# Optimization experiments

Measured on AMD Instinct MI355X. Metric: run time of the kernel, lower is better.

## Reference

```python
import jax, jax.numpy as jnp
import numpy as np

B, S, D, H = 2, 2048, 1024, 16
HD = D // H
MASK_VALUE = -1000000.0


def setup_inputs() -> dict:
    key = jax.random.key(0)
    ks = jax.random.split(key, 8)
    scale = 1.0 / np.sqrt(D)
    return {
        "Q": jax.random.normal(ks[0], (B, S, D), jnp.float32),
        "K": jax.random.normal(ks[1], (B, S, D), jnp.float32),
        "V": jax.random.normal(ks[2], (B, S, D), jnp.float32),
        "valid_lens": jax.random.randint(ks[3], (B,), 0, S).astype(jnp.int32),
        "Wq": jax.random.normal(ks[4], (D, D), jnp.float32) * scale,
        "Wk": jax.random.normal(ks[5], (D, D), jnp.float32) * scale,
        "Wv": jax.random.normal(ks[6], (D, D), jnp.float32) * scale,
        "Wo": jax.random.normal(ks[7], (D, D), jnp.float32) * scale,
    }


def _split_heads(x):
    # [B,S,D] -> [B,H,S,HD]
    return x.reshape(B, S, H, HD).transpose(0, 2, 1, 3)


def reference(Q, K, V, valid_lens, Wq, Wk, Wv, Wo):
    q = _split_heads(Q @ Wq)
    k = _split_heads(K @ Wk)
    v = _split_heads(V @ Wv)
    # scores: [B,H,Sq,Sk]
    scores = jnp.einsum("bhqd,bhkd->bhqk", q, k) / jnp.sqrt(jnp.float32(HD))
    # mask key positions >= valid_len (per batch, broadcast over heads/queries)
    key_pos = jnp.arange(S)  # [Sk]
    mask = key_pos[None, None, None, :] < valid_lens[:, None, None, None]
    scores = jnp.where(mask, scores, MASK_VALUE)
    attn = jax.nn.softmax(scores, axis=-1)
    out = jnp.einsum("bhqk,bhkd->bhqd", attn, v)  # [B,H,S,HD]
    out = out.transpose(0, 2, 1, 3).reshape(B, S, D)
    return out @ Wo
```

## Files before the change

### kernel.cpp

```cpp
#include <hip/hip_runtime.h>
#include <stdint.h>

#define B_ 2
#define S_ 2048
#define D_ 1024
#define H_ 16
#define HD_ 64
#define MG_ (B_*S_)
#define MASKV -1000000.0f
#define LP_ 72
#define LO_ 68
#define M2_ 17.3f
#define QSCALE_ (0.125f * 1.44269504088896f)

typedef __bf16 bf16;
typedef bf16 bf16x8 __attribute__((ext_vector_type(8)));
typedef bf16 bf16x4 __attribute__((ext_vector_type(4)));
typedef float f32x4 __attribute__((ext_vector_type(4)));

#define MFMA(a, b, c) __builtin_amdgcn_mfma_f32_16x16x32_bf16(a, b, c, 0, 0, 0)

__device__ __forceinline__ void gl_lds16(const bf16* g, bf16* l) {
  __builtin_amdgcn_global_load_lds((const __attribute__((address_space(1))) void*)g,
                                   (__attribute__((address_space(3))) void*)l, 16, 0, 0);
}

__global__ __launch_bounds__(256) void wcast_kernel(const float* __restrict__ W0, const float* __restrict__ W1,
                                                    const float* __restrict__ W2, const float* __restrict__ W3,
                                                    bf16* __restrict__ T) {
  const float* W = blockIdx.z == 0 ? W0 : blockIdx.z == 1 ? W1 : blockIdx.z == 2 ? W2 : W3;
  bf16* Tz = T + (size_t)blockIdx.z * D_ * D_;
  __shared__ float tile[32][33];
  int tx = threadIdx.x & 31, ty = threadIdx.x >> 5;
  int bn = blockIdx.x * 32, bk = blockIdx.y * 32;
#pragma unroll
  for (int i = 0; i < 32; i += 8)
    tile[ty + i][tx] = W[(size_t)(bk + ty + i) * D_ + bn + tx];
  __syncthreads();
#pragma unroll
  for (int i = 0; i < 32; i += 8)
    Tz[(size_t)(bn + ty + i) * D_ + bk + tx] = (bf16)tile[tx][ty + i];
}

__global__ __launch_bounds__(256) void qkvcast_kernel(const float* __restrict__ Qin, const float* __restrict__ Kin,
                                                      const float* __restrict__ Vin, bf16* __restrict__ qb,
                                                      bf16* __restrict__ kb, bf16* __restrict__ vb) {
  int t = blockIdx.y;
  const float* src = t == 0 ? Qin : t == 1 ? Kin : Vin;
  bf16* dst = t == 0 ? qb : t == 1 ? kb : vb;
  float sc = t == 0 ? QSCALE_ : 1.0f;
  size_t base4 = (size_t)blockIdx.x * 2048 + threadIdx.x;
#pragma unroll
  for (int j = 0; j < 8; ++j) {
    size_t i4 = base4 + (size_t)j * 256;
    float4 v = *(const float4*)&src[i4 * 4];
    bf16x4 bv; bv[0] = (bf16)(v.x * sc); bv[1] = (bf16)(v.y * sc);
    bv[2] = (bf16)(v.z * sc); bv[3] = (bf16)(v.w * sc);
    *(bf16x4*)&dst[i4 * 4] = bv;
  }
}

__global__ __launch_bounds__(256) void proj_gemm_b(const bf16* __restrict__ qb, const bf16* __restrict__ kb,
                                                   const bf16* __restrict__ vb, const bf16* __restrict__ WT,
                                                   bf16* __restrict__ qh, bf16* __restrict__ kh,
                                                   bf16* __restrict__ vT) {
  __shared__ alignas(16) bf16 Sa[128 * 32];
  __shared__ alignas(16) bf16 Sw[128 * 32];
  int mode = blockIdx.y;
  int bx = blockIdx.x;
  int i1 = (bx & 7) + ((bx >> 6) << 3);
  int i2 = (bx >> 3) & 7;
  int tid = threadIdx.x, lane = tid & 63, w = tid >> 6;
  int wm = w >> 1, wn = w & 1, ml = lane & 15, quad = lane >> 4;
  int l4 = lane >> 2, k8 = (lane & 3) * 8;
  f32x4 acc[4][4] = {};

  const bf16* Tok = mode == 0 ? qb : mode == 1 ? kb : vb;
  const bf16* Hp = WT + (size_t)mode * D_ * D_;
  int frow0 = i1 * 128, hrow0 = i2 * 128;
  bf16* Xs = (mode < 2) ? Sa : Sw;
  bf16* Ys = (mode < 2) ? Sw : Sa;

  for (int kk = 0; kk < D_; kk += 32) {
    __syncthreads();
#pragma unroll
    for (int j = 0; j < 2; ++j) {
      int chunk = w * 2 + j;
      gl_lds16(&Tok[(size_t)(frow0 + chunk * 16 + l4) * D_ + kk + k8], &Sa[chunk * 16 * 32]);
      gl_lds16(&Hp[(size_t)(hrow0 + chunk * 16 + l4) * D_ + kk + k8], &Sw[chunk * 16 * 32]);
    }
    __syncthreads();
    bf16x8 af[4], bfr[4];
#pragma unroll
    for (int mt = 0; mt < 4; ++mt) af[mt] = *(bf16x8*)&Xs[(wm * 64 + mt * 16 + ml) * 32 + quad * 8];
#pragma unroll
    for (int nt = 0; nt < 4; ++nt) bfr[nt] = *(bf16x8*)&Ys[(wn * 64 + nt * 16 + ml) * 32 + quad * 8];
#pragma unroll
    for (int mt = 0; mt < 4; ++mt)
#pragma unroll
      for (int nt = 0; nt < 4; ++nt)
        acc[mt][nt] = MFMA(af[mt], bfr[nt], acc[mt][nt]);
  }

  if (mode < 2) {
    bf16* dst = mode ? kh : qh;
    int m0 = i1 * 128, n0 = i2 * 128;
#pragma unroll
    for (int mt = 0; mt < 4; ++mt)
#pragma unroll
      for (int nt = 0; nt < 4; ++nt)
#pragma unroll
        for (int r = 0; r < 4; ++r) {
          int m = m0 + wm * 64 + mt * 16 + quad * 4 + r;
          int n = n0 + wn * 64 + nt * 16 + ml;
          int b = m >> 11, s = m & (S_ - 1), h = n >> 6, hd = n & 63;
          dst[(((size_t)(b * H_ + h)) * S_ + s) * HD_ + hd] = (bf16)acc[mt][nt][r];
        }
  } else {
    int m0 = i2 * 128, n0 = i1 * 128;
#pragma unroll
    for (int mt = 0; mt < 4; ++mt)
#pragma unroll
      for (int nt = 0; nt < 4; ++nt)
#pragma unroll
        for (int r = 0; r < 4; ++r) {
          int dcol = m0 + wm * 64 + mt * 16 + quad * 4 + r;
          int n = n0 + wn * 64 + nt * 16 + ml;
          int b = n >> 11, s = n & (S_ - 1), h = dcol >> 6, hd = dcol & 63;
          vT[(((size_t)(b * H_ + h)) * HD_ + hd) * S_ + s] = (bf16)acc[mt][nt][r];
        }
  }
}

__global__ __launch_bounds__(256) void proj_gemm(const float* __restrict__ Qin, const float* __restrict__ Kin,
                                                 const float* __restrict__ Vin, const bf16* __restrict__ WT,
                                                 bf16* __restrict__ qh, bf16* __restrict__ kh,
                                                 bf16* __restrict__ vT) {
  __shared__ alignas(16) bf16 Asf[128 * 32];
  __shared__ alignas(16) bf16 Ash[128 * 32];
  int mode = blockIdx.y;
  int bx = blockIdx.x;
  int i1 = (bx & 7) + ((bx >> 6) << 3);
  int i2 = (bx >> 3) & 7;
  int tid = threadIdx.x, lane = tid & 63, w = tid >> 6;
  int wm = w >> 1, wn = w & 1, ml = lane & 15, quad = lane >> 4;
  int rr = tid >> 3, c4 = (tid & 7) * 4;
  int l4 = lane >> 2, k8 = (lane & 3) * 8;
  f32x4 acc[4][4] = {};

  const float* Fp = mode == 0 ? Qin : mode == 1 ? Kin : Vin;
  const bf16* Hp = WT + (size_t)mode * D_ * D_;
  int frow0 = i1 * 128, hrow0 = i2 * 128;
  bf16* Xs = (mode < 2) ? Asf : Ash;
  bf16* Ys = (mode < 2) ? Ash : Asf;

  for (int kk = 0; kk < D_; kk += 32) {
    __syncthreads();
#pragma unroll
    for (int j = 0; j < 2; ++j) {
      int chunk = w * 2 + j;
      gl_lds16(&Hp[(size_t)(hrow0 + chunk * 16 + l4) * D_ + kk + k8], &Ash[chunk * 16 * 32]);
    }
#pragma unroll
    for (int p = 0; p < 4; ++p) {
      float4 v = *(const float4*)&Fp[(size_t)(frow0 + rr + p * 32) * D_ + kk + c4];
      bf16x4 bv; bv[0] = (bf16)v.x; bv[1] = (bf16)v.y; bv[2] = (bf16)v.z; bv[3] = (bf16)v.w;
      *(bf16x4*)&Asf[(rr + p * 32) * 32 + c4] = bv;
    }
    __syncthreads();
    bf16x8 af[4], bfr[4];
#pragma unroll
    for (int mt = 0; mt < 4; ++mt) af[mt] = *(bf16x8*)&Xs[(wm * 64 + mt * 16 + ml) * 32 + quad * 8];
#pragma unroll
    for (int nt = 0; nt < 4; ++nt) bfr[nt] = *(bf16x8*)&Ys[(wn * 64 + nt * 16 + ml) * 32 + quad * 8];
#pragma unroll
    for (int mt = 0; mt < 4; ++mt)
#pragma unroll
      for (int nt = 0; nt < 4; ++nt)
        acc[mt][nt] = MFMA(af[mt], bfr[nt], acc[mt][nt]);
  }

  if (mode < 2) {
    bf16* dst = mode ? kh : qh;
    float oscale = mode ? 1.0f : QSCALE_;
    int m0 = i1 * 128, n0 = i2 * 128;
#pragma unroll
    for (int mt = 0; mt < 4; ++mt)
#pragma unroll
      for (int nt = 0; nt < 4; ++nt)
#pragma unroll
        for (int r = 0; r < 4; ++r) {
          int m = m0 + wm * 64 + mt * 16 + quad * 4 + r;
          int n = n0 + wn * 64 + nt * 16 + ml;
          int b = m >> 11, s = m & (S_ - 1), h = n >> 6, hd = n & 63;
          dst[(((size_t)(b * H_ + h)) * S_ + s) * HD_ + hd] = (bf16)(acc[mt][nt][r] * oscale);
        }
  } else {
    int m0 = i2 * 128, n0 = i1 * 128;
#pragma unroll
    for (int mt = 0; mt < 4; ++mt)
#pragma unroll
      for (int nt = 0; nt < 4; ++nt)
#pragma unroll
        for (int r = 0; r < 4; ++r) {
          int dcol = m0 + wm * 64 + mt * 16 + quad * 4 + r;
          int n = n0 + wn * 64 + nt * 16 + ml;
          int b = n >> 11, s = n & (S_ - 1), h = dcol >> 6, hd = dcol & 63;
          vT[(((size_t)(b * H_ + h)) * HD_ + hd) * S_ + s] = (bf16)acc[mt][nt][r];
        }
  }
}

__global__ __launch_bounds__(256) void attn_kernel(const bf16* __restrict__ qh, const bf16* __restrict__ kh,
                                                   const bf16* __restrict__ vT, const int* __restrict__ vlen,
                                                   bf16* __restrict__ ctx) {
  __shared__ alignas(16) char ldsraw[35328];
  bf16* Ps = (bf16*)ldsraw;
  float* Om = (float*)ldsraw;
  float* Lv = (float*)(ldsraw + 34816);

  int tid = threadIdx.x, lane = tid & 63, w = tid >> 6;
  int ml = lane & 15, quad = lane >> 4;
  int wq = w >> 1, wk = w & 1;
  int bx = blockIdx.x;
  int bh = (bx & 7) + ((bx >> 8) << 3);
  int qt = (bx >> 3) & 31;
  int b = bh >> 4, h = bh & 15;
  const bf16* qbase = qh + ((size_t)bh * S_ + qt * 64 + wq * 32) * HD_;
  const bf16* kbase = kh + (size_t)bh * S_ * HD_;
  const bf16* vbase = vT + (size_t)bh * HD_ * S_;
  int valid = vlen[b];
  int nkt = (valid == 0) ? (S_ / 64) : ((valid + 63) >> 6);

  bf16x8 aq[2][2];
#pragma unroll
  for (int mt = 0; mt < 2; ++mt)
#pragma unroll
    for (int half = 0; half < 2; ++half)
      aq[mt][half] = *(const bf16x8*)&qbase[(mt * 16 + ml) * HD_ + half * 32 + quad * 8];

  bf16 onev = (bf16)1.0f;
  bf16x8 ones = {onev, onev, onev, onev, onev, onev, onev, onev};

  f32x4 o[2][4] = {};
  f32x4 lacc[2] = {};

  bf16* Pw = Ps + (size_t)w * 32 * LP_;

  for (int kt = wk; kt < nkt; kt += 2) {
    const bf16* kp = kbase + (size_t)kt * 64 * HD_;
    bool tail = (kt * 64 + 64 > valid);
    bf16x8 bk[4][2];
#pragma unroll
    for (int nt = 0; nt < 4; ++nt)
#pragma unroll
      for (int half = 0; half < 2; ++half)
        bk[nt][half] = *(const bf16x8*)&kp[(nt * 16 + ml) * HD_ + half * 32 + quad * 8];

#pragma unroll
    for (int mt = 0; mt < 2; ++mt) {
      f32x4 sc[4];
#pragma unroll
      for (int nt = 0; nt < 4; ++nt) {
        f32x4 c = {};
        c = MFMA(aq[mt][0], bk[nt][0], c);
        c = MFMA(aq[mt][1], bk[nt][1], c);
        sc[nt] = c;
      }
#pragma unroll
      for (int r = 0; r < 4; ++r) {
#pragma unroll
        for (int nt = 0; nt < 4; ++nt) {
          float s = sc[nt][r];
          if (tail) {
            int col = kt * 64 + nt * 16 + ml;
            if (col >= valid) s = MASKV;
          }
          if (valid == 0) s = 0.f;
          float p = exp2f(s - M2_);
          Pw[(mt * 16 + quad * 4 + r) * LP_ + nt * 16 + ml] = (bf16)p;
        }
      }
    }
#pragma unroll
    for (int ks = 0; ks < 2; ++ks) {
      bf16x8 bv[4];
#pragma unroll
      for (int ht = 0; ht < 4; ++ht)
        bv[ht] = *(const bf16x8*)&vbase[(size_t)(ht * 16 + ml) * S_ + kt * 64 + ks * 32 + quad * 8];
#pragma unroll
      for (int mt = 0; mt < 2; ++mt) {
        bf16x8 ap = *(bf16x8*)&Pw[(mt * 16 + ml) * LP_ + ks * 32 + quad * 8];
        lacc[mt] = MFMA(ap, ones, lacc[mt]);
#pragma unroll
        for (int ht = 0; ht < 4; ++ht) o[mt][ht] = MFMA(ap, bv[ht], o[mt][ht]);
      }
    }
  }

  __syncthreads();
#pragma unroll
  for (int mt = 0; mt < 2; ++mt) {
#pragma unroll
    for (int r = 0; r < 4; ++r) {
      int rl = mt * 16 + quad * 4 + r;
#pragma unroll
      for (int ht = 0; ht < 4; ++ht)
        Om[(w * 32 + rl) * LO_ + ht * 16 + ml] = o[mt][ht][r];
      if (ml == 0) Lv[w * 32 + rl] = lacc[mt][r];
    }
  }
  __syncthreads();
#pragma unroll 4
  for (int rr = 0; rr < 16; ++rr) {
    int rg = w * 16 + rr;
    int wqs = rg >> 5, rl = rg & 31;
    int s0 = (wqs * 2) * 32 + rl, s1 = (wqs * 2 + 1) * 32 + rl;
    float ls = Lv[s0] + Lv[s1];
    float ov = Om[s0 * LO_ + lane] + Om[s1 * LO_ + lane];
    ctx[((size_t)b * S_ + qt * 64 + rg) * D_ + h * 64 + lane] = (bf16)(ov / ls);
  }
}

__global__ __launch_bounds__(256) void out_gemm(const bf16* __restrict__ ctx, const bf16* __restrict__ WoT,
                                                float* __restrict__ out) {
  __shared__ alignas(16) bf16 As[128 * 32];
  __shared__ alignas(16) bf16 Bs[64 * 32];
  int bx = blockIdx.x;
  int mt8 = (bx & 7) + ((bx >> 7) << 3);
  int ntile = (bx >> 3) & 15;
  int tid = threadIdx.x, lane = tid & 63, w = tid >> 6;
  int wm = w >> 1, wn = w & 1, ml = lane & 15, quad = lane >> 4;
  int l4 = lane >> 2, k8 = (lane & 3) * 8;
  int m0 = mt8 * 128, n0 = ntile * 64;
  f32x4 acc[4][2] = {};
  for (int kk = 0; kk < D_; kk += 32) {
    __syncthreads();
#pragma unroll
    for (int j = 0; j < 2; ++j) {
      int chunk = w * 2 + j;
      gl_lds16(&ctx[(size_t)(m0 + chunk * 16 + l4) * D_ + kk + k8], &As[chunk * 16 * 32]);
    }
    gl_lds16(&WoT[(size_t)(n0 + w * 16 + l4) * D_ + kk + k8], &Bs[w * 16 * 32]);
    __syncthreads();
    bf16x8 af[4], bfr[2];
#pragma unroll
    for (int mt = 0; mt < 4; ++mt) af[mt] = *(bf16x8*)&As[(wm * 64 + mt * 16 + ml) * 32 + quad * 8];
#pragma unroll
    for (int nt = 0; nt < 2; ++nt) bfr[nt] = *(bf16x8*)&Bs[(wn * 32 + nt * 16 + ml) * 32 + quad * 8];
#pragma unroll
    for (int mt = 0; mt < 4; ++mt)
#pragma unroll
      for (int nt = 0; nt < 2; ++nt)
        acc[mt][nt] = MFMA(af[mt], bfr[nt], acc[mt][nt]);
  }
#pragma unroll
  for (int mt = 0; mt < 4; ++mt)
#pragma unroll
    for (int nt = 0; nt < 2; ++nt)
#pragma unroll
      for (int r = 0; r < 4; ++r) {
        int m = m0 + wm * 64 + mt * 16 + quad * 4 + r;
        int n = n0 + wn * 32 + nt * 16 + ml;
        out[(size_t)m * D_ + n] = acc[mt][nt][r];
      }
}

extern "C" void kernel_launch(void* const* d_in, const int* in_sizes, int n_in,
                              void* d_out, int out_size, void* d_ws, size_t ws_size,
                              hipStream_t stream) {
  const float* Q = (const float*)d_in[0];
  const float* K = (const float*)d_in[1];
  const float* V = (const float*)d_in[2];
  const int* vl = (const int*)d_in[3];
  const float* Wq = (const float*)d_in[4];
  const float* Wk = (const float*)d_in[5];
  const float* Wv = (const float*)d_in[6];
  const float* Wo = (const float*)d_in[7];
  char* ws = (char*)d_ws;
  bf16* WT  = (bf16*)ws;
  bf16* qh  = (bf16*)(ws + 8ull * 1024 * 1024);
  bf16* kh  = (bf16*)(ws + 16ull * 1024 * 1024);
  bf16* vT  = (bf16*)(ws + 24ull * 1024 * 1024);
  bf16* ctx = (bf16*)(ws + 32ull * 1024 * 1024);
  bf16* qb  = ctx;
  bf16* kb  = (bf16*)(ws + 40ull * 1024 * 1024);
  bf16* vb  = (bf16*)(ws + 48ull * 1024 * 1024);
  float* out = (float*)d_out;

  bool big = ws_size >= 56ull * 1024 * 1024;

  wcast_kernel<<<dim3(32, 32, 4), 256, 0, stream>>>(Wq, Wk, Wv, Wo, WT);
  if (big) {
    qkvcast_kernel<<<dim3(512, 3), 256, 0, stream>>>(Q, K, V, qb, kb, vb);
    proj_gemm_b<<<dim3(256, 3), 256, 0, stream>>>(qb, kb, vb, WT, qh, kh, vT);
  } else {
    proj_gemm<<<dim3(256, 3), 256, 0, stream>>>(Q, K, V, WT, qh, kh, vT);
  }
  attn_kernel<<<dim3(1024), 256, 0, stream>>>(qh, kh, vT, vl, ctx);
  out_gemm<<<dim3(512), 256, 0, stream>>>(ctx, WT + 3ull * D_ * D_, out);
}
```

Baseline: 222.9 us.

## Fuse weight and input casts into one kernel, skip K/V rows beyond valid length

Merges the weight transpose-cast and the Q/K/V bf16 cast into a single front kernel launch, removing one launch and letting both kinds of work share the GPU. The cast and the K/V projection GEMM now read valid_lens and skip token tiles past the rounded-up valid key length, since the attention kernel never reads those keys or values. This avoids wasted projection compute and memory traffic for masked keys, but relies on the attention kernel honouring the same kneed bound, including the valid==0 case treated as full length.

```diff
diff --git a/kernel.cpp b/kernel.cpp
--- a/kernel.cpp
+++ b/kernel.cpp
@@ -25,6 +25,130 @@
                                    (__attribute__((address_space(3))) void*)l, 16, 0, 0);
 }
 
+__device__ __forceinline__ int kneed_of(int valid) {
+  return (valid == 0) ? S_ : ((valid + 63) & ~63);
+}
+
+__global__ __launch_bounds__(256) void front_kernel(const float* __restrict__ W0, const float* __restrict__ W1,
+                                                    const float* __restrict__ W2, const float* __restrict__ W3,
+                                                    bf16* __restrict__ T, const float* __restrict__ Qin,
+                                                    const float* __restrict__ Kin, const float* __restrict__ Vin,
+                                                    bf16* __restrict__ qb, bf16* __restrict__ kb,
+                                                    bf16* __restrict__ vb, const int* __restrict__ vlen) {
+  __shared__ float tile[32][33];
+  int z = blockIdx.y;
+  if (z < 4) {
+    const float* W = z == 0 ? W0 : z == 1 ? W1 : z == 2 ? W2 : W3;
+    bf16* Tz = T + (size_t)z * D_ * D_;
+    int tx = threadIdx.x & 31, ty = threadIdx.x >> 5;
+    int bn = (blockIdx.x & 31) * 32, bk = (blockIdx.x >> 5) * 32;
+#pragma unroll
+    for (int i = 0; i < 32; i += 8)
+      tile[ty + i][tx] = W[(size_t)(bk + ty + i) * D_ + bn + tx];
+    __syncthreads();
+#pragma unroll
+    for (int i = 0; i < 32; i += 8)
+      Tz[(size_t)(bn + ty + i) * D_ + bk + tx] = (bf16)tile[tx][ty + i];
+  } else {
+    int t = z - 4;
+    const float* src = t == 0 ? Qin : t == 1 ? Kin : Vin;
+    bf16* dst = t == 0 ? qb : t == 1 ? kb : vb;
+    float sc = t == 0 ? QSCALE_ : 1.0f;
+    if (t) {
+      int m0 = blockIdx.x * 4;
+      int b = m0 >> 11, s0 = m0 & (S_ - 1);
+      int kneed128 = (kneed_of(vlen[b]) + 127) & ~127;
+      if (s0 >= kneed128) return;
+    }
+    size_t base4 = (size_t)blockIdx.x * 1024 + threadIdx.x;
+#pragma unroll
+    for (int j = 0; j < 4; ++j) {
+      size_t i4 = base4 + (size_t)j * 256;
+      float4 v = *(const float4*)&src[i4 * 4];
+      bf16x4 bv; bv[0] = (bf16)(v.x * sc); bv[1] = (bf16)(v.y * sc);
+      bv[2] = (bf16)(v.z * sc); bv[3] = (bf16)(v.w * sc);
+      *(bf16x4*)&dst[i4 * 4] = bv;
+    }
+  }
+}
+
+__global__ __launch_bounds__(256) void proj_gemm_b(const bf16* __restrict__ qb, const bf16* __restrict__ kb,
+                                                   const bf16* __restrict__ vb, const bf16* __restrict__ WT,
+                                                   bf16* __restrict__ qh, bf16* __restrict__ kh,
+                                                   bf16* __restrict__ vT, const int* __restrict__ vlen) {
+  __shared__ alignas(16) bf16 Sa[128 * 32];
+  __shared__ alignas(16) bf16 Sw[128 * 32];
+  int mode = blockIdx.y;
+  int bx = blockIdx.x;
+  int i1 = (bx & 7) + ((bx >> 6) << 3);
+  int i2 = (bx >> 3) & 7;
+  if (mode >= 1) {
+    int m0tok = i1 * 128;
+    int b = m0tok >> 11, s0 = m0tok & (S_ - 1);
+    if (s0 >= kneed_of(vlen[b])) return;
+  }
+  int tid = threadIdx.x, lane = tid & 63, w = tid >> 6;
+  int wm = w >> 1, wn = w & 1, ml = lane & 15, quad = lane >> 4;
+  int l4 = lane >> 2, k8 = (lane & 3) * 8;
+  f32x4 acc[4][4] = {};
+
+  const bf16* Tok = mode == 0 ? qb : mode == 1 ? kb : vb;
+  const bf16* Hp = WT + (size_t)mode * D_ * D_;
+  int frow0 = i1 * 128, hrow0 = i2 * 128;
+  bf16* Xs = (mode < 2) ? Sa : Sw;
+  bf16* Ys = (mode < 2) ? Sw : Sa;
+
+  for (int kk = 0; kk < D_; kk += 32) {
+    __syncthreads();
+#pragma unroll
+    for (int j = 0; j < 2; ++j) {
+      int chunk = w * 2 + j;
+      gl_lds16(&Tok[(size_t)(frow0 + chunk * 16 + l4) * D_ + kk + k8], &Sa[chunk * 16 * 32]);
+      gl_lds16(&Hp[(size_t)(hrow0 + chunk * 16 + l4) * D_ + kk + k8], &Sw[chunk * 16 * 32]);
+    }
+    __syncthreads();
+    bf16x8 af[4], bfr[4];
+#pragma unroll
+    for (int mt = 0; mt < 4; ++mt) af[mt] = *(bf16x8*)&Xs[(wm * 64 + mt * 16 + ml) * 32 + quad * 8];
+#pragma unroll
+    for (int nt = 0; nt < 4; ++nt) bfr[nt] = *(bf16x8*)&Ys[(wn * 64 + nt * 16 + ml) * 32 + quad * 8];
+#pragma unroll
+    for (int mt = 0; mt < 4; ++mt)
+#pragma unroll
+      for (int nt = 0; nt < 4; ++nt)
+        acc[mt][nt] = MFMA(af[mt], bfr[nt], acc[mt][nt]);
+  }
+
+  if (mode < 2) {
+    bf16* dst = mode ? kh : qh;
+    int m0 = i1 * 128, n0 = i2 * 128;
+#pragma unroll
+    for (int mt = 0; mt < 4; ++mt)
+#pragma unroll
+      for (int nt = 0; nt < 4; ++nt)
+#pragma unroll
+        for (int r = 0; r < 4; ++r) {
+          int m = m0 + wm * 64 + mt * 16 + quad * 4 + r;
+          int n = n0 + wn * 64 + nt * 16 + ml;
+          int b = m >> 11, s = m & (S_ - 1), h = n >> 6, hd = n & 63;
+          dst[(((size_t)(b * H_ + h)) * S_ + s) * HD_ + hd] = (bf16)acc[mt][nt][r];
+        }
+  } else {
+    int m0 = i2 * 128, n0 = i1 * 128;
+#pragma unroll
+    for (int mt = 0; mt < 4; ++mt)
+#pragma unroll
+      for (int nt = 0; nt < 4; ++nt)
+#pragma unroll
+        for (int r = 0; r < 4; ++r) {
+          int dcol = m0 + wm * 64 + mt * 16 + quad * 4 + r;
+          int n = n0 + wn * 64 + nt * 16 + ml;
+          int b = n >> 11, s = n & (S_ - 1), h = dcol >> 6, hd = dcol & 63;
+          vT[(((size_t)(b * H_ + h)) * HD_ + hd) * S_ + s] = (bf16)acc[mt][nt][r];
+        }
+  }
+}
+
 __global__ __launch_bounds__(256) void wcast_kernel(const float* __restrict__ W0, const float* __restrict__ W1,
                                                     const float* __restrict__ W2, const float* __restrict__ W3,
                                                     bf16* __restrict__ T) {
@@ -40,96 +164,6 @@
 #pragma unroll
   for (int i = 0; i < 32; i += 8)
     Tz[(size_t)(bn + ty + i) * D_ + bk + tx] = (bf16)tile[tx][ty + i];
-}
-
-__global__ __launch_bounds__(256) void qkvcast_kernel(const float* __restrict__ Qin, const float* __restrict__ Kin,
-                                                      const float* __restrict__ Vin, bf16* __restrict__ qb,
-                                                      bf16* __restrict__ kb, bf16* __restrict__ vb) {
-  int t = blockIdx.y;
-  const float* src = t == 0 ? Qin : t == 1 ? Kin : Vin;
-  bf16* dst = t == 0 ? qb : t == 1 ? kb : vb;
-  float sc = t == 0 ? QSCALE_ : 1.0f;
-  size_t base4 = (size_t)blockIdx.x * 2048 + threadIdx.x;
-#pragma unroll
-  for (int j = 0; j < 8; ++j) {
-    size_t i4 = base4 + (size_t)j * 256;
-    float4 v = *(const float4*)&src[i4 * 4];
-    bf16x4 bv; bv[0] = (bf16)(v.x * sc); bv[1] = (bf16)(v.y * sc);
-    bv[2] = (bf16)(v.z * sc); bv[3] = (bf16)(v.w * sc);
-    *(bf16x4*)&dst[i4 * 4] = bv;
-  }
-}
-
-__global__ __launch_bounds__(256) void proj_gemm_b(const bf16* __restrict__ qb, const bf16* __restrict__ kb,
-                                                   const bf16* __restrict__ vb, const bf16* __restrict__ WT,
-                                                   bf16* __restrict__ qh, bf16* __restrict__ kh,
-                                                   bf16* __restrict__ vT) {
-  __shared__ alignas(16) bf16 Sa[128 * 32];
-  __shared__ alignas(16) bf16 Sw[128 * 32];
-  int mode = blockIdx.y;
-  int bx = blockIdx.x;
-  int i1 = (bx & 7) + ((bx >> 6) << 3);
-  int i2 = (bx >> 3) & 7;
-  int tid = threadIdx.x, lane = tid & 63, w = tid >> 6;
-  int wm = w >> 1, wn = w & 1, ml = lane & 15, quad = lane >> 4;
-  int l4 = lane >> 2, k8 = (lane & 3) * 8;
-  f32x4 acc[4][4] = {};
-
-  const bf16* Tok = mode == 0 ? qb : mode == 1 ? kb : vb;
-  const bf16* Hp = WT + (size_t)mode * D_ * D_;
-  int frow0 = i1 * 128, hrow0 = i2 * 128;
-  bf16* Xs = (mode < 2) ? Sa : Sw;
-  bf16* Ys = (mode < 2) ? Sw : Sa;
-
-  for (int kk = 0; kk < D_; kk += 32) {
-    __syncthreads();
-#pragma unroll
-    for (int j = 0; j < 2; ++j) {
-      int chunk = w * 2 + j;
-      gl_lds16(&Tok[(size_t)(frow0 + chunk * 16 + l4) * D_ + kk + k8], &Sa[chunk * 16 * 32]);
-      gl_lds16(&Hp[(size_t)(hrow0 + chunk * 16 + l4) * D_ + kk + k8], &Sw[chunk * 16 * 32]);
-    }
-    __syncthreads();
-    bf16x8 af[4], bfr[4];
-#pragma unroll
-    for (int mt = 0; mt < 4; ++mt) af[mt] = *(bf16x8*)&Xs[(wm * 64 + mt * 16 + ml) * 32 + quad * 8];
-#pragma unroll
-    for (int nt = 0; nt < 4; ++nt) bfr[nt] = *(bf16x8*)&Ys[(wn * 64 + nt * 16 + ml) * 32 + quad * 8];
-#pragma unroll
-    for (int mt = 0; mt < 4; ++mt)
-#pragma unroll
-      for (int nt = 0; nt < 4; ++nt)
-        acc[mt][nt] = MFMA(af[mt], bfr[nt], acc[mt][nt]);
-  }
-
-  if (mode < 2) {
-    bf16* dst = mode ? kh : qh;
-    int m0 = i1 * 128, n0 = i2 * 128;
-#pragma unroll
-    for (int mt = 0; mt < 4; ++mt)
-#pragma unroll
-      for (int nt = 0; nt < 4; ++nt)
-#pragma unroll
-        for (int r = 0; r < 4; ++r) {
-          int m = m0 + wm * 64 + mt * 16 + quad * 4 + r;
-          int n = n0 + wn * 64 + nt * 16 + ml;
-          int b = m >> 11, s = m & (S_ - 1), h = n >> 6, hd = n & 63;
-          dst[(((size_t)(b * H_ + h)) * S_ + s) * HD_ + hd] = (bf16)acc[mt][nt][r];
-        }
-  } else {
-    int m0 = i2 * 128, n0 = i1 * 128;
-#pragma unroll
-    for (int mt = 0; mt < 4; ++mt)
-#pragma unroll
-      for (int nt = 0; nt < 4; ++nt)
-#pragma unroll
-        for (int r = 0; r < 4; ++r) {
-          int dcol = m0 + wm * 64 + mt * 16 + quad * 4 + r;
-          int n = n0 + wn * 64 + nt * 16 + ml;
-          int b = n >> 11, s = n & (S_ - 1), h = dcol >> 6, hd = dcol & 63;
-          vT[(((size_t)(b * H_ + h)) * HD_ + hd) * S_ + s] = (bf16)acc[mt][nt][r];
-        }
-  }
 }
 
 __global__ __launch_bounds__(256) void proj_gemm(const float* __restrict__ Qin, const float* __restrict__ Kin,
@@ -390,11 +424,11 @@
 
   bool big = ws_size >= 56ull * 1024 * 1024;
 
-  wcast_kernel<<<dim3(32, 32, 4), 256, 0, stream>>>(Wq, Wk, Wv, Wo, WT);
   if (big) {
-    qkvcast_kernel<<<dim3(512, 3), 256, 0, stream>>>(Q, K, V, qb, kb, vb);
-    proj_gemm_b<<<dim3(256, 3), 256, 0, stream>>>(qb, kb, vb, WT, qh, kh, vT);
+    front_kernel<<<dim3(1024, 7), 256, 0, stream>>>(Wq, Wk, Wv, Wo, WT, Q, K, V, qb, kb, vb, vl);
+    proj_gemm_b<<<dim3(256, 3), 256, 0, stream>>>(qb, kb, vb, WT, qh, kh, vT, vl);
   } else {
+    wcast_kernel<<<dim3(32, 32, 4), 256, 0, stream>>>(Wq, Wk, Wv, Wo, WT);
     proj_gemm<<<dim3(256, 3), 256, 0, stream>>>(Q, K, V, WT, qh, kh, vT);
   }
   attn_kernel<<<dim3(1024), 256, 0, stream>>>(qh, kh, vT, vl, ctx);
```

After: 216.0 us, median of 3. 1.03x faster.
